# Kernel tuning notes

Hardware: AMD Instinct MI355X
Metric: run time of the kernel (lower is better)

## Reference

```python
import jax, jax.numpy as jnp
import numpy as np

B, T, D, N, R = 2, 2048, 1024, 16, 64  # batch, seqlen, d_model, d_state, dt_rank


def setup_inputs() -> dict:
    key = jax.random.key(0)
    ks = jax.random.split(key, 8)
    sc = 0.02  # init scale for weights
    return {
        "x": jax.random.normal(ks[0], (B, T, D), jnp.float32),
        "W_in": jax.random.normal(ks[1], (2 * D, D), jnp.float32) * sc,   # in_proj.weight
        "conv_w": jax.random.normal(ks[2], (D, 3), jnp.float32) * sc,     # conv1d.weight [D,1,3] squeezed
        "W_x": jax.random.normal(ks[3], (R + 2 * N, D), jnp.float32) * sc, # x_proj.weight
        "W_dt": jax.random.normal(ks[4], (D, R), jnp.float32) * sc,        # dt_proj.weight
        "b_dt": jnp.ones((D,), jnp.float32),                               # dt_proj.bias (init 1.0)
        "A_log": jnp.full((D, N), -2.0, jnp.float32),                      # A_log (filled -2.0)
        "D_param": jnp.ones((D,), jnp.float32),                            # D skip
        "W_C": jax.random.normal(ks[5], (D, N), jnp.float32) * sc,         # C_proj.weight
        "W_out": jax.random.normal(ks[6], (D, D), jnp.float32) * sc,       # out_proj.weight
    }


def reference(x, W_in, conv_w, W_x, W_dt, b_dt, A_log, D_param, W_C, W_out):
    # in_proj -> chunk into (x, z)
    xz = jnp.einsum('btd,ed->bte', x, W_in)           # [B,T,2D]
    xc, z = jnp.split(xz, 2, axis=-1)                 # [B,T,D] each

    # depthwise conv1d, kernel 3, padding 1, no bias
    xp = jnp.pad(xc, ((0, 0), (1, 1), (0, 0)))
    xconv = (xp[:, :-2] * conv_w[:, 0]
             + xp[:, 1:-1] * conv_w[:, 1]
             + xp[:, 2:] * conv_w[:, 2])              # [B,T,D]
    xs = jax.nn.silu(xconv)

    # x_proj -> split dt / B / C params
    x_dbl = jnp.einsum('btd,ed->bte', xs, W_x)        # [B,T,R+2N]
    dt_param = x_dbl[..., :R]
    Bp = x_dbl[..., R:R + N]                          # [B,T,N]
    Cp = x_dbl[..., R + N:]                           # [B,T,N]

    dt = jax.nn.softplus(dt_param @ W_dt.T + b_dt) + 1e-5  # [B,T,D]

    # discretization
    A_disc = jnp.exp(-jnp.exp(A_log)[None, None] * dt[..., None])  # [B,T,D,N]
    Bx = Bp[:, :, None, :] * dt[..., None] * xs[..., None]         # [B,T,D,N]
    C = Cp @ W_C.T                                                  # [B,T,D]

    # selective scan: s_t = A_t * s_{t-1} + B_t * x_t;  y_t = C_t * sum_n s_t
    def step(s, inp):
        A_t, Bx_t = inp
        s = A_t * s + Bx_t
        return s, s.sum(-1)                           # carry [B,D,N], out [B,D]

    s0 = jnp.zeros((x.shape[0], D, N), x.dtype)
    _, ssum = jax.lax.scan(step, s0,
                           (A_disc.transpose(1, 0, 2, 3), Bx.transpose(1, 0, 2, 3)))
    ssum = ssum.transpose(1, 0, 2)                    # [B,T,D]

    y = C * ssum + D_param * xs                       # [B,T,D]
    return jnp.einsum('btd,ed->bte', y, W_out) * jax.nn.silu(z)
```

## Files before the change

kernel.cpp:

```cpp
#include <hip/hip_runtime.h>

typedef unsigned short u16;
typedef __attribute__((ext_vector_type(4))) float f4;
typedef __attribute__((ext_vector_type(4))) unsigned short us4;
typedef __attribute__((ext_vector_type(8))) unsigned short us8;
typedef __attribute__((ext_vector_type(8))) short s8v;
typedef __attribute__((ext_vector_type(4))) float f32x4;
typedef __attribute__((ext_vector_type(4))) unsigned int u4v;

#define DEVI __device__ __forceinline__

DEVI u16 f2bf(float f) {
  unsigned u = __float_as_uint(f);
  u = (u + 0x7FFFu + ((u >> 16) & 1u)) >> 16;
  return (u16)u;
}
DEVI float bf2f(u16 v) { return __uint_as_float(((unsigned)v) << 16); }
DEVI float siluf(float x) { return x / (1.f + __expf(-x)); }

__global__ void k_cvt_all(const float* __restrict__ x, const float* __restrict__ w1,
                          const float* __restrict__ wo, const float* __restrict__ wdt,
                          const float* __restrict__ wx,
                          u16* __restrict__ xb, u16* __restrict__ w1b,
                          u16* __restrict__ wob, u16* __restrict__ wdtb,
                          u16* __restrict__ wxb) {
  const int blk = blockIdx.x;
  const int tid = threadIdx.x;
  if (blk >= 7232) {
    int i = (blk - 7232) * 256 + tid;
    int row = i >> 8;
    us4 o;
    if (row < 96) {
      f4 v = ((const f4*)wx)[i];
#pragma unroll
      for (int j = 0; j < 4; ++j) o[j] = f2bf(v[j]);
    } else {
      o[0] = 0; o[1] = 0; o[2] = 0; o[3] = 0;
    }
    ((us4*)wxb)[i] = o;
    return;
  }
  const float* src; u16* dst; int i;
  if (blk < 4096)      { src = x;   dst = xb;   i = blk * 256 + tid; }
  else if (blk < 6144) { src = w1;  dst = w1b;  i = (blk - 4096) * 256 + tid; }
  else if (blk < 7168) { src = wo;  dst = wob;  i = (blk - 6144) * 256 + tid; }
  else                 { src = wdt; dst = wdtb; i = (blk - 7168) * 256 + tid; }
  f4 v = ((const f4*)src)[i];
  us4 o;
#pragma unroll
  for (int j = 0; j < 4; ++j) o[j] = f2bf(v[j]);
  ((us4*)dst)[i] = o;
}

template <int EPI>
__global__ __launch_bounds__(512, 2)
void k_gemm_bt(const u16* __restrict__ A, int lda,
               const u16* __restrict__ B, int ldb,
               float* __restrict__ C, int ldc, int nvalid,
               int K, int kchunk, size_t zstride, int lognx,
               const float* __restrict__ bvec,
               const u16* __restrict__ zsrc,
               u16* __restrict__ ob1, u16* __restrict__ ob2) {
  __shared__ __align__(16) char smem[32768];
  const int tid = threadIdx.x;
  const int wave = tid >> 6, lane = tid & 63;

  const int nwg = gridDim.x * gridDim.y;
  int bid = blockIdx.y * gridDim.x + blockIdx.x;
  {
    const int cpx = nwg >> 3;
    bid = (bid & 7) * cpx + (bid >> 3);
  }
  const int mBase = (bid >> lognx) << 7;
  const int nBase = (bid & ((1 << lognx) - 1)) << 7;
  const int kbeg = blockIdx.z * kchunk;
  int kend = kbeg + kchunk; if (kend > K) kend = K;
  if (EPI == 4) ob1 += (size_t)blockIdx.z * zstride;
  else          C   += (size_t)blockIdx.z * zstride;

  const int wr = wave >> 2, wc = wave & 3;
  const int row0 = tid >> 2, kg = tid & 3;

  const u16* Ag = A + (size_t)(mBase + row0) * lda + kg * 8;
  const u16* Bg = B + (size_t)(nBase + row0) * ldb + kg * 8;
  char* ldsA0 = smem + wave * 1024;
  char* ldsA1 = smem + 8192 + wave * 1024;
  char* ldsB0 = smem + 16384 + wave * 1024;
  char* ldsB1 = smem + 24576 + wave * 1024;
  const u16* As = (const u16*)smem;
  const u16* Bs = (const u16*)(smem + 16384);

  const int fr = lane & 15, fk = (lane >> 4) << 3;
  const int aoff = ((wr << 6) + fr) * 32 + fk;
  const int boff = ((wc << 5) + fr) * 32 + fk;

  f32x4 acc[4][2];
#pragma unroll
  for (int m = 0; m < 4; ++m)
#pragma unroll
    for (int n = 0; n < 2; ++n) acc[m][n] = {0.f, 0.f, 0.f, 0.f};

  for (int k0 = kbeg; k0 < kend; k0 += 64) {
    __syncthreads();
    __builtin_amdgcn_global_load_lds((const __attribute__((address_space(1))) void*)(Ag + k0),
                                     (__attribute__((address_space(3))) void*)(ldsA0), 16, 0, 0);
    __builtin_amdgcn_global_load_lds((const __attribute__((address_space(1))) void*)(Ag + k0 + 32),
                                     (__attribute__((address_space(3))) void*)(ldsA1), 16, 0, 0);
    __builtin_amdgcn_global_load_lds((const __attribute__((address_space(1))) void*)(Bg + k0),
                                     (__attribute__((address_space(3))) void*)(ldsB0), 16, 0, 0);
    __builtin_amdgcn_global_load_lds((const __attribute__((address_space(1))) void*)(Bg + k0 + 32),
                                     (__attribute__((address_space(3))) void*)(ldsB1), 16, 0, 0);
    __syncthreads();
#pragma unroll
    for (int kk = 0; kk < 2; ++kk) {
      const u16* Ap = As + (kk << 12);
      const u16* Bp = Bs + (kk << 12);
      s8v av[4], bv[2];
#pragma unroll
      for (int m = 0; m < 4; ++m) av[m] = *(const s8v*)(Ap + aoff + (m << 9));
#pragma unroll
      for (int n = 0; n < 2; ++n) bv[n] = *(const s8v*)(Bp + boff + (n << 9));
#pragma unroll
      for (int m = 0; m < 4; ++m)
#pragma unroll
        for (int n = 0; n < 2; ++n)
          acc[m][n] = __builtin_amdgcn_mfma_f32_16x16x32_bf16(av[m], bv[n], acc[m][n], 0, 0, 0);
    }
  }

  if (EPI == 2) {
    u16* ct = (u16*)smem;
    const int r16 = (lane >> 4) << 2;
    __syncthreads();
#pragma unroll
    for (int m = 0; m < 4; ++m)
#pragma unroll
      for (int n = 0; n < 2; ++n)
#pragma unroll
        for (int j = 0; j < 4; ++j)
          ct[((wr << 6) + (m << 4) + r16 + j) * 128 + (wc << 5) + (n << 4) + fr] =
              f2bf(acc[m][n][j]);
    __syncthreads();
    u16* dst = (nBase < 1024) ? ob1 : ob2;
    const int ncol = nBase & 1023;
#pragma unroll
    for (int it = 0; it < 4; ++it) {
      const int s = it * 512 + tid;
      const int tr = s >> 4, colq = (s & 15) << 3;
      *(us8*)(dst + ((size_t)(mBase + tr) << 10) + ncol + colq) =
          *(const us8*)(ct + tr * 128 + colq);
    }
    return;
  }

  const int crow0 = mBase + (wr << 6) + ((lane >> 4) << 2);
  const int ccol0 = nBase + (wc << 5) + (lane & 15);
#pragma unroll
  for (int m = 0; m < 4; ++m) {
#pragma unroll
    for (int n = 0; n < 2; ++n) {
      const int cc = ccol0 + (n << 4);
      if (cc < nvalid) {
#pragma unroll
        for (int j = 0; j < 4; ++j) {
          const int rr = crow0 + (m << 4) + j;
          float v = acc[m][n][j];
          if (EPI == 0) {
            C[(size_t)rr * ldc + cc] = v;
          } else if (EPI == 1) {
            v *= siluf(bf2f(zsrc[((size_t)rr << 10) + cc]));
            C[(size_t)rr * ldc + cc] = v;
          } else if (EPI == 3) {
            float pre = v + bvec[cc];
            float dtv = (pre > 20.f ? pre : __logf(1.f + __expf(pre))) + 1e-5f;
            ob1[((size_t)rr << 10) + cc] = f2bf(dtv);
          } else {
            ob1[(size_t)rr * ldc + cc] = f2bf(v);
          }
        }
      }
    }
  }
}

__global__ void k_red8(const u16* __restrict__ parts, float* __restrict__ xdbl,
                       u16* __restrict__ xdblb) {
  const int i = blockIdx.x * 256 + threadIdx.x;
  f4 s = {0.f, 0.f, 0.f, 0.f};
#pragma unroll
  for (int z = 0; z < 8; ++z) {
    us4 v = ((const us4*)(parts + (size_t)z * 393216))[i];
#pragma unroll
    for (int j = 0; j < 4; ++j) s[j] += bf2f(v[j]);
  }
  ((f4*)xdbl)[i] = s;
  us4 o;
#pragma unroll
  for (int j = 0; j < 4; ++j) o[j] = f2bf(s[j]);
  ((us4*)xdblb)[i] = o;
}

__global__ void k_conv2(const u16* __restrict__ xcb, const float* __restrict__ conv_w,
                        u16* __restrict__ xsb) {
  const int b = blockIdx.x >> 8;
  const int t0 = (blockIdx.x & 255) << 3;
  const int d = threadIdx.x << 2;
  const u16* base = xcb + ((size_t)b * 2048 << 10) + d;
  const f4* cw = (const f4*)(conv_w + d * 3);
  f4 c0 = cw[0], c1 = cw[1], c2 = cw[2];
  const float w[12] = {c0[0], c0[1], c0[2], c0[3], c1[0], c1[1], c1[2], c1[3],
                       c2[0], c2[1], c2[2], c2[3]};
  const f4 zero = {0.f, 0.f, 0.f, 0.f};
  auto ld = [&](int t) -> f4 {
    us4 v = *(const us4*)(base + ((size_t)t << 10));
    f4 r;
#pragma unroll
    for (int j = 0; j < 4; ++j) r[j] = bf2f(v[j]);
    return r;
  };
  f4 prev = (t0 == 0) ? zero : ld(t0 - 1);
  f4 cur = ld(t0);
#pragma unroll
  for (int i = 0; i < 8; ++i) {
    const int t = t0 + i;
    f4 nxt = (t == 2047) ? zero : ld(t + 1);
    us4 xbv;
#pragma unroll
    for (int j = 0; j < 4; ++j) {
      float xc = prev[j] * w[j * 3] + cur[j] * w[j * 3 + 1] + nxt[j] * w[j * 3 + 2];
      xbv[j] = f2bf(siluf(xc));
    }
    *(us4*)(xsb + ((size_t)(b * 2048 + t) << 10) + d) = xbv;
    prev = cur; cur = nxt;
  }
}

__global__ void k_scanA(const u16* __restrict__ dtb, const u16* __restrict__ xsb,
                        const float* __restrict__ xdbl, const float* __restrict__ A_log,
                        unsigned* __restrict__ PS) {
  __shared__ float bxs[32][16];
  const int tid = threadIdx.x;
  const int d = (blockIdx.x << 8) + tid;
  const int c = blockIdx.y;
  const int b = blockIdx.z;
  const int btBase = (b << 11) + (c << 5);
  for (int i = tid; i < 512; i += 256) {
    bxs[i >> 4][i & 15] = xdbl[(size_t)(btBase + (i >> 4)) * 96 + 64 + (i & 15)];
  }
  float a[16];
  {
    const f4* al = (const f4*)(A_log + d * 16);
#pragma unroll
    for (int q = 0; q < 4; ++q) {
      f4 v = al[q];
#pragma unroll
      for (int j = 0; j < 4; ++j) a[q * 4 + j] = -__expf(v[j]);
    }
  }
  bool uni = true;
#pragma unroll
  for (int n = 1; n < 16; ++n) uni = uni && (a[n] == a[0]);
  __syncthreads();
  float P[16], S[16];
#pragma unroll
  for (int n = 0; n < 16; ++n) { P[n] = 1.f; S[n] = 0.f; }
  if (uni) {
    const float a0 = a[0];
    float Pu = 1.f;
    for (int tau = 0; tau < 32; ++tau) {
      const size_t bt = btBase + tau;
      const float dt = bf2f(dtb[(bt << 10) + d]);
      const float dx = dt * bf2f(xsb[(bt << 10) + d]);
      const float Av = __expf(a0 * dt);
      Pu *= Av;
#pragma unroll
      for (int n = 0; n < 16; ++n) S[n] = fmaf(Av, S[n], bxs[tau][n] * dx);
    }
#pragma unroll
    for (int n = 0; n < 16; ++n) P[n] = Pu;
  } else {
    for (int tau = 0; tau < 32; ++tau) {
      const size_t bt = btBase + tau;
      const float dt = bf2f(dtb[(bt << 10) + d]);
      const float dx = dt * bf2f(xsb[(bt << 10) + d]);
#pragma unroll
      for (int n = 0; n < 16; ++n) {
        const float Av = __expf(a[n] * dt);
        P[n] *= Av;
        S[n] = fmaf(Av, S[n], bxs[tau][n] * dx);
      }
    }
  }
  const size_t base = (size_t)(((b << 6) + c) * 1024 + d) << 4;
#pragma unroll
  for (int q = 0; q < 4; ++q) {
    u4v pk;
#pragma unroll
    for (int j = 0; j < 4; ++j) {
      pk[j] = (unsigned)f2bf(P[q * 4 + j]) | ((unsigned)f2bf(S[q * 4 + j]) << 16);
    }
    *(u4v*)(PS + base + q * 4) = pk;
  }
}

__global__ void k_scanB(const unsigned* __restrict__ PS, u16* __restrict__ SI) {
  const int i = (blockIdx.x << 8) + threadIdx.x;
  const int n = i & 15;
  const int dd = (i >> 4) & 1023;
  const int b = i >> 14;
  float s = 0.f;
  for (int c = 0; c < 64; ++c) {
    const size_t idx = ((size_t)(((b << 6) + c) * 1024 + dd) << 4) + n;
    const unsigned w = PS[idx];
    SI[idx] = f2bf(s);
    s = fmaf(bf2f((u16)(w & 0xFFFF)), s, bf2f((u16)(w >> 16)));
  }
}

__global__ void k_scanC(const u16* __restrict__ dtb, const u16* __restrict__ xsb,
                        const float* __restrict__ xdbl, const float* __restrict__ A_log,
                        const u16* __restrict__ SI, const float* __restrict__ W_C,
                        const float* __restrict__ D_param, u16* __restrict__ yb) {
  __shared__ float bxs[32][32];
  const int tid = threadIdx.x;
  const int d = (blockIdx.x << 8) + tid;
  const int c = blockIdx.y;
  const int b = blockIdx.z;
  const int btBase = (b << 11) + (c << 5);
  for (int i = tid; i < 1024; i += 256) {
    bxs[i >> 5][i & 31] = xdbl[(size_t)(btBase + (i >> 5)) * 96 + 64 + (i & 31)];
  }
  float a[16], wc[16];
  {
    const f4* al = (const f4*)(A_log + d * 16);
    const f4* wcp = (const f4*)(W_C + d * 16);
#pragma unroll
    for (int q = 0; q < 4; ++q) {
      f4 v = al[q], u = wcp[q];
#pragma unroll
      for (int j = 0; j < 4; ++j) { a[q * 4 + j] = -__expf(v[j]); wc[q * 4 + j] = u[j]; }
    }
  }
  bool uni = true;
#pragma unroll
  for (int n = 1; n < 16; ++n) uni = uni && (a[n] == a[0]);
  const float Dp = D_param[d];
  float s[16];
  const size_t base = (size_t)(((b << 6) + c) * 1024 + d) << 4;
#pragma unroll
  for (int q = 0; q < 4; ++q) {
    us4 v = *(const us4*)(SI + base + q * 4);
#pragma unroll
    for (int j = 0; j < 4; ++j) s[q * 4 + j] = bf2f(v[j]);
  }
  __syncthreads();
  if (uni) {
    const float a0 = a[0];
    for (int tau = 0; tau < 32; ++tau) {
      const size_t bt = btBase + tau;
      const float dt = bf2f(dtb[(bt << 10) + d]);
      const float xs = bf2f(xsb[(bt << 10) + d]);
      const float dx = dt * xs;
      const float Av = __expf(a0 * dt);
      float ssum = 0.f, cp = 0.f;
#pragma unroll
      for (int n = 0; n < 16; ++n) {
        s[n] = fmaf(Av, s[n], bxs[tau][n] * dx);
        ssum += s[n];
        cp = fmaf(bxs[tau][16 + n], wc[n], cp);
      }
      const float y = fmaf(cp, ssum, Dp * xs);
      yb[(bt << 10) + d] = f2bf(y);
    }
  } else {
    for (int tau = 0; tau < 32; ++tau) {
      const size_t bt = btBase + tau;
      const float dt = bf2f(dtb[(bt << 10) + d]);
      const float xs = bf2f(xsb[(bt << 10) + d]);
      const float dx = dt * xs;
      float ssum = 0.f, cp = 0.f;
#pragma unroll
      for (int n = 0; n < 16; ++n) {
        const float Av = __expf(a[n] * dt);
        s[n] = fmaf(Av, s[n], bxs[tau][n] * dx);
        ssum += s[n];
        cp = fmaf(bxs[tau][16 + n], wc[n], cp);
      }
      const float y = fmaf(cp, ssum, Dp * xs);
      yb[(bt << 10) + d] = f2bf(y);
    }
  }
}

extern "C" void kernel_launch(void* const* d_in, const int* in_sizes, int n_in,
                              void* d_out, int out_size, void* d_ws, size_t ws_size,
                              hipStream_t stream) {
  const float* x     = (const float*)d_in[0];
  const float* W_in  = (const float*)d_in[1];
  const float* convw = (const float*)d_in[2];
  const float* W_x   = (const float*)d_in[3];
  const float* W_dt  = (const float*)d_in[4];
  const float* b_dt  = (const float*)d_in[5];
  const float* A_log = (const float*)d_in[6];
  const float* D_par = (const float*)d_in[7];
  const float* W_C   = (const float*)d_in[8];
  const float* W_out = (const float*)d_in[9];
  float* out = (float*)d_out;
  (void)in_sizes; (void)n_in; (void)out_size; (void)ws_size;

  char* w = (char*)d_ws;
  auto take = [&](size_t bytes) { char* p = w; w += (bytes + 255) & ~(size_t)255; return p; };
  u16* xb     = (u16*)take(8388608);
  u16* w1b    = (u16*)take(4194304);
  u16* wxb    = (u16*)take(262144);
  u16* wob    = (u16*)take(2097152);
  u16* wdtb   = (u16*)take(131072);
  u16* xdblb  = (u16*)take(786432);
  u16* yb     = (u16*)take(8388608);
  u16* xsb    = (u16*)take(8388608);
  u16* xcb    = (u16*)take(8388608);
  u16* zb     = (u16*)take(8388608);
  u16* dtb    = (u16*)take(8388608);
  u16* xdblp  = (u16*)take(6291456);
  float* xdbl = (float*)take(1572864);
  unsigned* PS= (unsigned*)take(8388608);
  u16* SI     = (u16*)take(4194304);

  k_cvt_all<<<7360, 256, 0, stream>>>(x, W_in, W_out, W_dt, W_x,
                                      xb, w1b, wob, wdtb, wxb);
  dim3 g1(16, 32, 1);
  k_gemm_bt<2><<<g1, 512, 0, stream>>>(xb, 1024, w1b, 1024, nullptr, 0, 2048,
                                       1024, 1024, 0, 4, nullptr, nullptr, xcb, zb);
  k_conv2<<<512, 256, 0, stream>>>(xcb, convw, xsb);
  dim3 g2(1, 32, 8);
  k_gemm_bt<4><<<g2, 512, 0, stream>>>(xsb, 1024, wxb, 1024, nullptr, 96, 96,
                                       1024, 128, 393216, 0, nullptr, nullptr, xdblp, nullptr);
  k_red8<<<384, 256, 0, stream>>>(xdblp, xdbl, xdblb);
  dim3 g4(8, 32, 1);
  k_gemm_bt<3><<<g4, 512, 0, stream>>>(xdblb, 96, wdtb, 64, nullptr, 0, 1024,
                                       64, 64, 0, 3, b_dt, nullptr, dtb, nullptr);
  dim3 gs(4, 64, 2);
  k_scanA<<<gs, 256, 0, stream>>>(dtb, xsb, xdbl, A_log, PS);
  k_scanB<<<128, 256, 0, stream>>>(PS, SI);
  k_scanC<<<gs, 256, 0, stream>>>(dtb, xsb, xdbl, A_log, SI, W_C, D_par, yb);
  dim3 g3(8, 32, 1);
  k_gemm_bt<1><<<g3, 512, 0, stream>>>(yb, 1024, wob, 1024, out, 1024, 1024,
                                       1024, 1024, 0, 3, nullptr, zb, nullptr, nullptr);
}
```

Measured before the change: 123.7 us.

## Fuse depthwise conv+SiLU into in_proj GEMM epilogue and drop fp32 xdbl copy

The in_proj GEMM epilogue now computes the 3-tap depthwise conv and SiLU directly from the bf16 tile held in shared memory and writes xs for interior rows. It still writes the raw xc only for the two edge rows at each end of a tile. A small fix-up kernel then computes xs for the tile-boundary rows that need neighbours from other tiles. Separately, the fp32 xdbl buffer is removed, so the scan kernels read B/C parameters from the bf16 copy. This saves a full conv pass over xc and one fp32 write, at the cost of bf16 precision for B/C and a heavier GEMM epilogue.

Result: no change. 124.3 us (+0.5%).

```diff
diff --git a/kernel.cpp b/kernel.cpp
--- a/kernel.cpp
+++ b/kernel.cpp
@@ -60,7 +60,8 @@
                int K, int kchunk, size_t zstride, int lognx,
                const float* __restrict__ bvec,
                const u16* __restrict__ zsrc,
-               u16* __restrict__ ob1, u16* __restrict__ ob2) {
+               u16* __restrict__ ob1, u16* __restrict__ ob2,
+               const float* __restrict__ cw, u16* __restrict__ ob3) {
   __shared__ __align__(16) char smem[32768];
   const int tid = threadIdx.x;
   const int wave = tid >> 6, lane = tid & 63;
@@ -141,14 +142,38 @@
           ct[((wr << 6) + (m << 4) + r16 + j) * 128 + (wc << 5) + (n << 4) + fr] =
               f2bf(acc[m][n][j]);
     __syncthreads();
-    u16* dst = (nBase < 1024) ? ob1 : ob2;
-    const int ncol = nBase & 1023;
-#pragma unroll
-    for (int it = 0; it < 4; ++it) {
-      const int s = it * 512 + tid;
-      const int tr = s >> 4, colq = (s & 15) << 3;
-      *(us8*)(dst + ((size_t)(mBase + tr) << 10) + ncol + colq) =
-          *(const us8*)(ct + tr * 128 + colq);
+    if (nBase >= 1024) {
+      const int ncol = nBase - 1024;
+#pragma unroll
+      for (int it = 0; it < 4; ++it) {
+        const int s = it * 512 + tid;
+        const int tr = s >> 4, colq = (s & 15) << 3;
+        *(us8*)(ob2 + ((size_t)(mBase + tr) << 10) + ncol + colq) =
+            *(const us8*)(ct + tr * 128 + colq);
+      }
+    } else {
+      const int ncol = nBase;
+#pragma unroll
+      for (int it = 0; it < 4; ++it) {
+        const int s = it * 512 + tid;
+        const int tr = s >> 4, colq = (s & 15) << 3;
+        us8 curv = *(const us8*)(ct + tr * 128 + colq);
+        if (tr < 2 || tr > 125)
+          *(us8*)(ob1 + ((size_t)(mBase + tr) << 10) + ncol + colq) = curv;
+        if (tr >= 1 && tr <= 126) {
+          us8 lft = *(const us8*)(ct + (tr - 1) * 128 + colq);
+          us8 rgt = *(const us8*)(ct + (tr + 1) * 128 + colq);
+          const float* cwp = cw + (ncol + colq) * 3;
+          us8 o;
+#pragma unroll
+          for (int j = 0; j < 8; ++j) {
+            float xcv = bf2f(lft[j]) * cwp[j * 3] + bf2f(curv[j]) * cwp[j * 3 + 1] +
+                        bf2f(rgt[j]) * cwp[j * 3 + 2];
+            o[j] = f2bf(siluf(xcv));
+          }
+          *(us8*)(ob3 + ((size_t)(mBase + tr) << 10) + ncol + colq) = o;
+        }
+      }
     }
     return;
   }
@@ -183,60 +208,53 @@
   }
 }
 
-__global__ void k_red8(const u16* __restrict__ parts, float* __restrict__ xdbl,
-                       u16* __restrict__ xdblb) {
-  const int i = blockIdx.x * 256 + threadIdx.x;
-  f4 s = {0.f, 0.f, 0.f, 0.f};
-#pragma unroll
-  for (int z = 0; z < 8; ++z) {
-    us4 v = ((const us4*)(parts + (size_t)z * 393216))[i];
-#pragma unroll
-    for (int j = 0; j < 4; ++j) s[j] += bf2f(v[j]);
-  }
-  ((f4*)xdbl)[i] = s;
-  us4 o;
-#pragma unroll
-  for (int j = 0; j < 4; ++j) o[j] = f2bf(s[j]);
-  ((us4*)xdblb)[i] = o;
-}
-
-__global__ void k_conv2(const u16* __restrict__ xcb, const float* __restrict__ conv_w,
-                        u16* __restrict__ xsb) {
-  const int b = blockIdx.x >> 8;
-  const int t0 = (blockIdx.x & 255) << 3;
+__global__ void k_conv_fix(const u16* __restrict__ xcb, const float* __restrict__ conv_w,
+                           u16* __restrict__ xsb) {
+  const int k = blockIdx.x >> 1;
+  const int bt = (k << 7) + ((blockIdx.x & 1) ? 127 : 0);
+  const int t = bt & 2047;
   const int d = threadIdx.x << 2;
-  const u16* base = xcb + ((size_t)b * 2048 << 10) + d;
-  const f4* cw = (const f4*)(conv_w + d * 3);
-  f4 c0 = cw[0], c1 = cw[1], c2 = cw[2];
-  const float w[12] = {c0[0], c0[1], c0[2], c0[3], c1[0], c1[1], c1[2], c1[3],
-                       c2[0], c2[1], c2[2], c2[3]};
-  const f4 zero = {0.f, 0.f, 0.f, 0.f};
-  auto ld = [&](int t) -> f4 {
-    us4 v = *(const us4*)(base + ((size_t)t << 10));
+  auto ld = [&](int row) -> f4 {
+    us4 v = *(const us4*)(xcb + ((size_t)row << 10) + d);
     f4 r;
 #pragma unroll
     for (int j = 0; j < 4; ++j) r[j] = bf2f(v[j]);
     return r;
   };
-  f4 prev = (t0 == 0) ? zero : ld(t0 - 1);
-  f4 cur = ld(t0);
-#pragma unroll
-  for (int i = 0; i < 8; ++i) {
-    const int t = t0 + i;
-    f4 nxt = (t == 2047) ? zero : ld(t + 1);
-    us4 xbv;
-#pragma unroll
-    for (int j = 0; j < 4; ++j) {
-      float xc = prev[j] * w[j * 3] + cur[j] * w[j * 3 + 1] + nxt[j] * w[j * 3 + 2];
-      xbv[j] = f2bf(siluf(xc));
-    }
-    *(us4*)(xsb + ((size_t)(b * 2048 + t) << 10) + d) = xbv;
-    prev = cur; cur = nxt;
-  }
+  const f4 zero = {0.f, 0.f, 0.f, 0.f};
+  f4 l = (t > 0) ? ld(bt - 1) : zero;
+  f4 c = ld(bt);
+  f4 r = (t < 2047) ? ld(bt + 1) : zero;
+  const f4* cwq = (const f4*)(conv_w + d * 3);
+  f4 c0 = cwq[0], c1 = cwq[1], c2 = cwq[2];
+  const float w[12] = {c0[0], c0[1], c0[2], c0[3], c1[0], c1[1], c1[2], c1[3],
+                       c2[0], c2[1], c2[2], c2[3]};
+  us4 o;
+#pragma unroll
+  for (int j = 0; j < 4; ++j) {
+    float xcv = l[j] * w[j * 3] + c[j] * w[j * 3 + 1] + r[j] * w[j * 3 + 2];
+    o[j] = f2bf(siluf(xcv));
+  }
+  *(us4*)(xsb + ((size_t)bt << 10) + d) = o;
+}
+
+__global__ void k_red8(const u16* __restrict__ parts, u16* __restrict__ xdblb) {
+  const int i = blockIdx.x * 256 + threadIdx.x;
+  f4 s = {0.f, 0.f, 0.f, 0.f};
+#pragma unroll
+  for (int z = 0; z < 8; ++z) {
+    us4 v = ((const us4*)(parts + (size_t)z * 393216))[i];
+#pragma unroll
+    for (int j = 0; j < 4; ++j) s[j] += bf2f(v[j]);
+  }
+  us4 o;
+#pragma unroll
+  for (int j = 0; j < 4; ++j) o[j] = f2bf(s[j]);
+  ((us4*)xdblb)[i] = o;
 }
 
 __global__ void k_scanA(const u16* __restrict__ dtb, const u16* __restrict__ xsb,
-                        const float* __restrict__ xdbl, const float* __restrict__ A_log,
+                        const u16* __restrict__ xdblb, const float* __restrict__ A_log,
                         unsigned* __restrict__ PS) {
   __shared__ float bxs[32][16];
   const int tid = threadIdx.x;
@@ -245,7 +263,7 @@
   const int b = blockIdx.z;
   const int btBase = (b << 11) + (c << 5);
   for (int i = tid; i < 512; i += 256) {
-    bxs[i >> 4][i & 15] = xdbl[(size_t)(btBase + (i >> 4)) * 96 + 64 + (i & 15)];
+    bxs[i >> 4][i & 15] = bf2f(xdblb[(size_t)(btBase + (i >> 4)) * 96 + 64 + (i & 15)]);
   }
   float a[16];
   {
@@ -318,7 +336,7 @@
 }
 
 __global__ void k_scanC(const u16* __restrict__ dtb, const u16* __restrict__ xsb,
-                        const float* __restrict__ xdbl, const float* __restrict__ A_log,
+                        const u16* __restrict__ xdblb, const float* __restrict__ A_log,
                         const u16* __restrict__ SI, const float* __restrict__ W_C,
                         const float* __restrict__ D_param, u16* __restrict__ yb) {
   __shared__ float bxs[32][32];
@@ -328,7 +346,7 @@
   const int b = blockIdx.z;
   const int btBase = (b << 11) + (c << 5);
   for (int i = tid; i < 1024; i += 256) {
-    bxs[i >> 5][i & 31] = xdbl[(size_t)(btBase + (i >> 5)) * 96 + 64 + (i & 31)];
+    bxs[i >> 5][i & 31] = bf2f(xdblb[(size_t)(btBase + (i >> 5)) * 96 + 64 + (i & 31)]);
   }
   float a[16], wc[16];
   {
@@ -422,7 +440,6 @@
   u16* zb     = (u16*)take(8388608);
   u16* dtb    = (u16*)take(8388608);
   u16* xdblp  = (u16*)take(6291456);
-  float* xdbl = (float*)take(1572864);
   unsigned* PS= (unsigned*)take(8388608);
   u16* SI     = (u16*)take(4194304);
 
@@ -430,20 +447,24 @@
                                       xb, w1b, wob, wdtb, wxb);
   dim3 g1(16, 32, 1);
   k_gemm_bt<2><<<g1, 512, 0, stream>>>(xb, 1024, w1b, 1024, nullptr, 0, 2048,
-                                       1024, 1024, 0, 4, nullptr, nullptr, xcb, zb);
-  k_conv2<<<512, 256, 0, stream>>>(xcb, convw, xsb);
+                                       1024, 1024, 0, 4, nullptr, nullptr, xcb, zb,
+                                       convw, xsb);
+  k_conv_fix<<<64, 256, 0, stream>>>(xcb, convw, xsb);
   dim3 g2(1, 32, 8);
   k_gemm_bt<4><<<g2, 512, 0, stream>>>(xsb, 1024, wxb, 1024, nullptr, 96, 96,
-                                       1024, 128, 393216, 0, nullptr, nullptr, xdblp, nullptr);
-  k_red8<<<384, 256, 0, stream>>>(xdblp, xdbl, xdblb);
+                                       1024, 128, 393216, 0, nullptr, nullptr, xdblp, nullptr,
+                                       nullptr, nullptr);
+  k_red8<<<384, 256, 0, stream>>>(xdblp, xdblb);
   dim3 g4(8, 32, 1);
   k_gemm_bt<3><<<g4, 512, 0, stream>>>(xdblb, 96, wdtb, 64, nullptr, 0, 1024,
-                                       64, 64, 0, 3, b_dt, nullptr, dtb, nullptr);
+                                       64, 64, 0, 3, b_dt, nullptr, dtb, nullptr,
+                                       nullptr, nullptr);
   dim3 gs(4, 64, 2);
-  k_scanA<<<gs, 256, 0, stream>>>(dtb, xsb, xdbl, A_log, PS);
+  k_scanA<<<gs, 256, 0, stream>>>(dtb, xsb, xdblb, A_log, PS);
   k_scanB<<<128, 256, 0, stream>>>(PS, SI);
-  k_scanC<<<gs, 256, 0, stream>>>(dtb, xsb, xdbl, A_log, SI, W_C, D_par, yb);
+  k_scanC<<<gs, 256, 0, stream>>>(dtb, xsb, xdblb, A_log, SI, W_C, D_par, yb);
   dim3 g3(8, 32, 1);
   k_gemm_bt<1><<<g3, 512, 0, stream>>>(yb, 1024, wob, 1024, out, 1024, 1024,
-                                       1024, 1024, 0, 3, nullptr, zb, nullptr, nullptr);
-}
+                                       1024, 1024, 0, 3, nullptr, zb, nullptr, nullptr,
+                                       nullptr, nullptr);
+}
```
